# Kernel tuning notes

Measured on AMD Instinct MI355X. Metric: run time of the kernel, lower is better.

The kernel has to match this reference:

```python
import jax, jax.numpy as jnp
import numpy as np

D_IN = 200   # 4 * d_embeddings
H = 64       # hidden_size

def setup_inputs() -> dict:
    key = jax.random.key(0)
    ks = jax.random.split(key, 7)
    B, T = 4096, 128
    s_ih = 1.0 / np.sqrt(H)
    x = jax.random.normal(ks[0], (B, T, D_IN), dtype=jnp.float32)
    W_ih = jax.random.uniform(ks[1], (H, D_IN), minval=-s_ih, maxval=s_ih, dtype=jnp.float32)
    W_hh = jax.random.uniform(ks[2], (H, H), minval=-s_ih, maxval=s_ih, dtype=jnp.float32)
    b_ih = jax.random.uniform(ks[3], (H,), minval=-s_ih, maxval=s_ih, dtype=jnp.float32)
    b_hh = jax.random.uniform(ks[4], (H,), minval=-s_ih, maxval=s_ih, dtype=jnp.float32)
    W_out = jax.random.uniform(ks[5], (1, H), minval=-s_ih, maxval=s_ih, dtype=jnp.float32)
    b_out = jax.random.uniform(ks[6], (1,), minval=-s_ih, maxval=s_ih, dtype=jnp.float32)
    return {"x": x, "W_ih": W_ih, "W_hh": W_hh, "b_ih": b_ih, "b_hh": b_hh,
            "W_out": W_out, "b_out": b_out}

def reference(x, W_ih, W_hh, b_ih, b_hh, W_out, b_out):
    B = x.shape[0]
    # precompute input projection for all timesteps: [B, T, H]
    xp = jnp.einsum('btd,hd->bth', x, W_ih) + b_ih + b_hh
    def step(h, xt):
        h = jnp.tanh(xt + h @ W_hh.T)
        return h, None
    h0 = jnp.zeros((B, H), dtype=x.dtype)
    h_last, _ = jax.lax.scan(step, h0, jnp.swapaxes(xp, 0, 1))  # scan over time
    return jax.nn.sigmoid(h_last @ W_out.T + b_out)  # [B, 1]
```

## Files before the change

kernel.cpp:

```cpp
#include <hip/hip_runtime.h>
#include <hip/hip_bf16.h>


#define TSEQ 128
#define DIN  200
#define HID  64
#define NB   16
#define TC   4
#define NCH  (TSEQ/TC)

typedef short bf16x8 __attribute__((ext_vector_type(8)));
typedef float f32x4  __attribute__((ext_vector_type(4)));

__device__ __forceinline__ short f2bf(float f) {
  __hip_bfloat16 h = __float2bfloat16(f);
  return __builtin_bit_cast(short, h);
}
__device__ __forceinline__ bf16x8 cvt8(f32x4 a, f32x4 b) {
  bf16x8 r;
#pragma unroll
  for (int i = 0; i < 4; ++i) { r[i] = f2bf(a[i]); r[4 + i] = f2bf(b[i]); }
  return r;
}
__device__ __forceinline__ float fast_tanh(float x) {
  x = fminf(10.f, fmaxf(-10.f, x));
  float e = __expf(2.f * x);
  return (e - 1.f) * __builtin_amdgcn_rcpf(e + 1.f);
}
__device__ __forceinline__ void barrier_lds() {
  asm volatile("s_waitcnt lgkmcnt(0)" ::: "memory");
  __builtin_amdgcn_s_barrier();
  asm volatile("" ::: "memory");
}

__global__ __launch_bounds__(256, 1) void rnn_fused(
    const float* __restrict__ x,   const float* __restrict__ Wih,
    const float* __restrict__ Whh, const float* __restrict__ bih,
    const float* __restrict__ bhh, const float* __restrict__ Wout,
    const float* __restrict__ bout, float* __restrict__ out)
{
  __shared__ float          xp[TC][NB][68];
  __shared__ unsigned short hbuf[2][NB][72];

  const int tid  = threadIdx.x;
  const int w    = tid >> 6;
  const int lane = tid & 63;
  const int m    = lane & 15;
  const int g    = lane >> 4;
  const int b0   = blockIdx.x * NB;

  f32x4 pre[7][2];
  {
    const float* xrow = x + ((size_t)(b0 + m) * TSEQ + w) * DIN;
#pragma unroll
    for (int ks = 0; ks < 7; ++ks) {
      const int d = ks * 32 + g * 8;
      if (d < DIN) {
        pre[ks][0] = *reinterpret_cast<const f32x4*>(xrow + d);
        pre[ks][1] = *reinterpret_cast<const f32x4*>(xrow + d + 4);
      } else {
        pre[ks][0] = (f32x4)0.f; pre[ks][1] = (f32x4)0.f;
      }
    }
  }

  bf16x8 wihf[4][7];
#pragma unroll
  for (int nt = 0; nt < 4; ++nt) {
    const float* wr = Wih + (size_t)(nt * 16 + m) * DIN;
#pragma unroll
    for (int ks = 0; ks < 7; ++ks) {
      const int d = ks * 32 + g * 8;
      if (d < DIN) {
        f32x4 u0 = *reinterpret_cast<const f32x4*>(wr + d);
        f32x4 u1 = *reinterpret_cast<const f32x4*>(wr + d + 4);
        wihf[nt][ks] = cvt8(u0, u1);
      } else {
        wihf[nt][ks] = (bf16x8)0;
      }
    }
  }
  bf16x8 whhf[2];
#pragma unroll
  for (int ks = 0; ks < 2; ++ks) {
    const float* wr = Whh + (size_t)(w * 16 + m) * HID + ks * 32 + g * 8;
    f32x4 u0 = *reinterpret_cast<const f32x4*>(wr);
    f32x4 u1 = *reinterpret_cast<const f32x4*>(wr + 4);
    whhf[ks] = cvt8(u0, u1);
  }
  float bias[4];
#pragma unroll
  for (int nt = 0; nt < 4; ++nt) bias[nt] = bih[nt * 16 + m] + bhh[nt * 16 + m];

  for (int i = tid; i < NB * 72; i += 256) hbuf[1][0][i] = 0;
  barrier_lds();

  for (int c = 0; c < NCH; ++c) {
    bf16x8 afr[7];
#pragma unroll
    for (int ks = 0; ks < 7; ++ks) afr[ks] = cvt8(pre[ks][0], pre[ks][1]);

    if (c + 1 < NCH) {
      const float* xrow = x + ((size_t)(b0 + m) * TSEQ + ((c + 1) * TC + w)) * DIN;
#pragma unroll
      for (int ks = 0; ks < 7; ++ks) {
        const int d = ks * 32 + g * 8;
        if (d < DIN) {
          pre[ks][0] = *reinterpret_cast<const f32x4*>(xrow + d);
          pre[ks][1] = *reinterpret_cast<const f32x4*>(xrow + d + 4);
        }
      }
    }

    f32x4 acc[4];
#pragma unroll
    for (int nt = 0; nt < 4; ++nt) acc[nt] = (f32x4)(bias[nt]);
#pragma unroll
    for (int ks = 0; ks < 7; ++ks)
#pragma unroll
      for (int nt = 0; nt < 4; ++nt)
        acc[nt] = __builtin_amdgcn_mfma_f32_16x16x32_bf16(afr[ks], wihf[nt][ks], acc[nt], 0, 0, 0);

#pragma unroll
    for (int nt = 0; nt < 4; ++nt)
#pragma unroll
      for (int r = 0; r < 4; ++r)
        xp[w][g * 4 + r][nt * 16 + m] = acc[nt][r];
    barrier_lds();

#pragma unroll
    for (int tl = 0; tl < TC; ++tl) {
      const int tt = c * TC + tl;
      const int rb = tt & 1, pb = rb ^ 1;

      bf16x8 ha0 = *reinterpret_cast<const bf16x8*>(&hbuf[pb][m][g * 8]);
      bf16x8 ha1 = *reinterpret_cast<const bf16x8*>(&hbuf[pb][m][32 + g * 8]);

      f32x4 racc;
#pragma unroll
      for (int r = 0; r < 4; ++r) racc[r] = xp[tl][g * 4 + r][w * 16 + m];

      racc = __builtin_amdgcn_mfma_f32_16x16x32_bf16(ha0, whhf[0], racc, 0, 0, 0);
      racc = __builtin_amdgcn_mfma_f32_16x16x32_bf16(ha1, whhf[1], racc, 0, 0, 0);

#pragma unroll
      for (int r = 0; r < 4; ++r) {
        const float hv = fast_tanh(racc[r]);
        hbuf[rb][g * 4 + r][w * 16 + m] = (unsigned short)f2bf(hv);
        if (tt == TSEQ - 1) xp[0][g * 4 + r][w * 16 + m] = hv;
      }
      barrier_lds();
    }
  }

  if (tid < 64) {
    const int b = m, q = g;
    float s = 0.f;
#pragma unroll
    for (int j = 0; j < 16; ++j) s += xp[0][b][q * 16 + j] * Wout[q * 16 + j];
    s += __shfl_xor(s, 16, 64);
    s += __shfl_xor(s, 32, 64);
    if (q == 0) {
      const float z = s + bout[0];
      out[b0 + b] = 1.f / (1.f + __expf(-z));
    }
  }
}

extern "C" void kernel_launch(void* const* d_in, const int* in_sizes, int n_in,
                              void* d_out, int out_size, void* d_ws, size_t ws_size,
                              hipStream_t stream) {
  const float* x    = (const float*)d_in[0];
  const float* Wih  = (const float*)d_in[1];
  const float* Whh  = (const float*)d_in[2];
  const float* bih  = (const float*)d_in[3];
  const float* bhh  = (const float*)d_in[4];
  const float* Wout = (const float*)d_in[5];
  const float* bout = (const float*)d_in[6];
  float* out = (float*)d_out;

  const int B = in_sizes[0] / (TSEQ * DIN);
  rnn_fused<<<dim3(B / NB), dim3(256), 0, stream>>>(x, Wih, Whh, bih, bhh, Wout, bout, out);
}
```

Measured before the change: 101.6 us.

## Give each wavefront its own batch rows to drop block barriers; deepen x prefetch

Each wavefront now owns 4 batch rows and runs the full 64-wide recurrence itself, instead of four waves sharing 16 rows. Hidden state and the projected inputs stay in wave-private LDS, so every per-timestep block barrier goes away. The cost is 8 recurrent MFMAs per step instead of 2, with 3/4 of the A rows duplicated. The x loads are double-buffered two chunks ahead, tanh is rewritten as exp2 plus rcp, and the output reduction uses shuffles only.

```diff
diff --git a/kernel.cpp b/kernel.cpp
--- a/kernel.cpp
+++ b/kernel.cpp
@@ -5,7 +5,6 @@
 #define TSEQ 128
 #define DIN  200
 #define HID  64
-#define NB   16
 #define TC   4
 #define NCH  (TSEQ/TC)
 
@@ -22,15 +21,10 @@
   for (int i = 0; i < 4; ++i) { r[i] = f2bf(a[i]); r[4 + i] = f2bf(b[i]); }
   return r;
 }
-__device__ __forceinline__ float fast_tanh(float x) {
-  x = fminf(10.f, fmaxf(-10.f, x));
-  float e = __expf(2.f * x);
-  return (e - 1.f) * __builtin_amdgcn_rcpf(e + 1.f);
-}
-__device__ __forceinline__ void barrier_lds() {
-  asm volatile("s_waitcnt lgkmcnt(0)" ::: "memory");
-  __builtin_amdgcn_s_barrier();
-  asm volatile("" ::: "memory");
+__device__ __forceinline__ float tanh_fast(float x) {
+  float e = exp2f(x * 2.885390081777927f);
+  float r = __builtin_amdgcn_rcpf(1.f + e);
+  return __builtin_fmaf(-2.f, r, 1.f);
 }
 
 __global__ __launch_bounds__(256, 1) void rnn_fused(
@@ -39,30 +33,34 @@
     const float* __restrict__ bhh, const float* __restrict__ Wout,
     const float* __restrict__ bout, float* __restrict__ out)
 {
-  __shared__ float          xp[TC][NB][68];
-  __shared__ unsigned short hbuf[2][NB][72];
+  __shared__ float          xps[4][TC][HID][4];
+  __shared__ unsigned short hb [4][4][HID];
 
   const int tid  = threadIdx.x;
   const int w    = tid >> 6;
   const int lane = tid & 63;
   const int m    = lane & 15;
   const int g    = lane >> 4;
-  const int b0   = blockIdx.x * NB;
+  const int bw   = blockIdx.x * 16 + w * 4;
 
-  f32x4 pre[7][2];
-  {
-    const float* xrow = x + ((size_t)(b0 + m) * TSEQ + w) * DIN;
+  const float* xrow = x + ((size_t)(bw + (m >> 2)) * TSEQ + (m & 3)) * DIN;
+
+  f32x4 pA[7][2], pB[7][2];
+  auto LOADC = [&](f32x4 (&P)[7][2], int c) {
+    const float* p = xrow + (size_t)c * (TC * DIN);
 #pragma unroll
     for (int ks = 0; ks < 7; ++ks) {
       const int d = ks * 32 + g * 8;
-      if (d < DIN) {
-        pre[ks][0] = *reinterpret_cast<const f32x4*>(xrow + d);
-        pre[ks][1] = *reinterpret_cast<const f32x4*>(xrow + d + 4);
+      if (d + 8 <= DIN) {
+        P[ks][0] = *reinterpret_cast<const f32x4*>(p + d);
+        P[ks][1] = *reinterpret_cast<const f32x4*>(p + d + 4);
       } else {
-        pre[ks][0] = (f32x4)0.f; pre[ks][1] = (f32x4)0.f;
+        P[ks][0] = (f32x4)0.f; P[ks][1] = (f32x4)0.f;
       }
     }
-  }
+  };
+  LOADC(pA, 0);
+  LOADC(pB, 1);
 
   bf16x8 wihf[4][7];
 #pragma unroll
@@ -71,50 +69,42 @@
 #pragma unroll
     for (int ks = 0; ks < 7; ++ks) {
       const int d = ks * 32 + g * 8;
-      if (d < DIN) {
-        f32x4 u0 = *reinterpret_cast<const f32x4*>(wr + d);
-        f32x4 u1 = *reinterpret_cast<const f32x4*>(wr + d + 4);
-        wihf[nt][ks] = cvt8(u0, u1);
-      } else {
+      if (d + 8 <= DIN)
+        wihf[nt][ks] = cvt8(*reinterpret_cast<const f32x4*>(wr + d),
+                            *reinterpret_cast<const f32x4*>(wr + d + 4));
+      else
         wihf[nt][ks] = (bf16x8)0;
-      }
     }
   }
-  bf16x8 whhf[2];
+  bf16x8 whhf[4][2];
 #pragma unroll
-  for (int ks = 0; ks < 2; ++ks) {
-    const float* wr = Whh + (size_t)(w * 16 + m) * HID + ks * 32 + g * 8;
-    f32x4 u0 = *reinterpret_cast<const f32x4*>(wr);
-    f32x4 u1 = *reinterpret_cast<const f32x4*>(wr + 4);
-    whhf[ks] = cvt8(u0, u1);
-  }
-  float bias[4];
+  for (int nt = 0; nt < 4; ++nt)
 #pragma unroll
-  for (int nt = 0; nt < 4; ++nt) bias[nt] = bih[nt * 16 + m] + bhh[nt * 16 + m];
+    for (int hf = 0; hf < 2; ++hf) {
+      const float* wr = Whh + (size_t)(nt * 16 + m) * HID + hf * 32 + g * 8;
+      whhf[nt][hf] = cvt8(*reinterpret_cast<const f32x4*>(wr),
+                          *reinterpret_cast<const f32x4*>(wr + 4));
+    }
+  float biasv[4];
+#pragma unroll
+  for (int nt = 0; nt < 4; ++nt) biasv[nt] = bih[nt * 16 + m] + bhh[nt * 16 + m];
+  const float woutv = Wout[g * 16 + m];
+  const float bout0 = bout[0];
 
-  for (int i = tid; i < NB * 72; i += 256) hbuf[1][0][i] = 0;
-  barrier_lds();
+  reinterpret_cast<unsigned int*>(&hb[w][0][0])[lane]      = 0u;
+  reinterpret_cast<unsigned int*>(&hb[w][0][0])[lane + 64] = 0u;
 
-  for (int c = 0; c < NCH; ++c) {
+  float vf[4];
+
+  auto BODY = [&](f32x4 (&P)[7][2], int c) {
     bf16x8 afr[7];
 #pragma unroll
-    for (int ks = 0; ks < 7; ++ks) afr[ks] = cvt8(pre[ks][0], pre[ks][1]);
-
-    if (c + 1 < NCH) {
-      const float* xrow = x + ((size_t)(b0 + m) * TSEQ + ((c + 1) * TC + w)) * DIN;
-#pragma unroll
-      for (int ks = 0; ks < 7; ++ks) {
-        const int d = ks * 32 + g * 8;
-        if (d < DIN) {
-          pre[ks][0] = *reinterpret_cast<const f32x4*>(xrow + d);
-          pre[ks][1] = *reinterpret_cast<const f32x4*>(xrow + d + 4);
-        }
-      }
-    }
+    for (int ks = 0; ks < 7; ++ks) afr[ks] = cvt8(P[ks][0], P[ks][1]);
+    if (c + 2 < NCH) LOADC(P, c + 2);
 
     f32x4 acc[4];
 #pragma unroll
-    for (int nt = 0; nt < 4; ++nt) acc[nt] = (f32x4)(bias[nt]);
+    for (int nt = 0; nt < 4; ++nt) acc[nt] = (f32x4)(biasv[nt]);
 #pragma unroll
     for (int ks = 0; ks < 7; ++ks)
 #pragma unroll
@@ -124,46 +114,51 @@
 #pragma unroll
     for (int nt = 0; nt < 4; ++nt)
 #pragma unroll
-      for (int r = 0; r < 4; ++r)
-        xp[w][g * 4 + r][nt * 16 + m] = acc[nt][r];
-    barrier_lds();
+      for (int rr = 0; rr < 4; ++rr)
+        xps[w][rr][nt * 16 + m][g] = acc[nt][rr];
 
 #pragma unroll
     for (int tl = 0; tl < TC; ++tl) {
-      const int tt = c * TC + tl;
-      const int rb = tt & 1, pb = rb ^ 1;
-
-      bf16x8 ha0 = *reinterpret_cast<const bf16x8*>(&hbuf[pb][m][g * 8]);
-      bf16x8 ha1 = *reinterpret_cast<const bf16x8*>(&hbuf[pb][m][32 + g * 8]);
-
-      f32x4 racc;
+      f32x4 racc[4];
 #pragma unroll
-      for (int r = 0; r < 4; ++r) racc[r] = xp[tl][g * 4 + r][w * 16 + m];
-
-      racc = __builtin_amdgcn_mfma_f32_16x16x32_bf16(ha0, whhf[0], racc, 0, 0, 0);
-      racc = __builtin_amdgcn_mfma_f32_16x16x32_bf16(ha1, whhf[1], racc, 0, 0, 0);
-
+      for (int nt = 0; nt < 4; ++nt)
+        racc[nt] = *reinterpret_cast<const f32x4*>(&xps[w][tl][nt * 16 + m][0]);
+      bf16x8 ha0 = *reinterpret_cast<const bf16x8*>(&hb[w][m & 3][g * 8]);
+      bf16x8 ha1 = *reinterpret_cast<const bf16x8*>(&hb[w][m & 3][32 + g * 8]);
+#pragma unroll
+      for (int nt = 0; nt < 4; ++nt) {
+        racc[nt] = __builtin_amdgcn_mfma_f32_16x16x32_bf16(ha0, whhf[nt][0], racc[nt], 0, 0, 0);
+        racc[nt] = __builtin_amdgcn_mfma_f32_16x16x32_bf16(ha1, whhf[nt][1], racc[nt], 0, 0, 0);
+      }
 #pragma unroll
       for (int r = 0; r < 4; ++r) {
-        const float hv = fast_tanh(racc[r]);
-        hbuf[rb][g * 4 + r][w * 16 + m] = (unsigned short)f2bf(hv);
-        if (tt == TSEQ - 1) xp[0][g * 4 + r][w * 16 + m] = hv;
+        float v = (g == 0) ? racc[0][r] : (g == 1) ? racc[1][r]
+                 : (g == 2) ? racc[2][r] : racc[3][r];
+        v = tanh_fast(v);
+        vf[r] = v;
+        hb[w][r][g * 16 + m] = (unsigned short)f2bf(v);
       }
-      barrier_lds();
     }
+  };
+
+  for (int c = 0; c < NCH; c += 2) { BODY(pA, c); BODY(pB, c + 1); }
+
+  f32x4 s;
+#pragma unroll
+  for (int r = 0; r < 4; ++r) s[r] = vf[r] * woutv;
+#pragma unroll
+  for (int mask = 1; mask < 64; mask <<= 1) {
+#pragma unroll
+    for (int r = 0; r < 4; ++r) s[r] += __shfl_xor(s[r], mask, 64);
   }
-
-  if (tid < 64) {
-    const int b = m, q = g;
-    float s = 0.f;
+  if (lane == 0) {
+    f32x4 o;
 #pragma unroll
-    for (int j = 0; j < 16; ++j) s += xp[0][b][q * 16 + j] * Wout[q * 16 + j];
-    s += __shfl_xor(s, 16, 64);
-    s += __shfl_xor(s, 32, 64);
-    if (q == 0) {
-      const float z = s + bout[0];
-      out[b0 + b] = 1.f / (1.f + __expf(-z));
+    for (int r = 0; r < 4; ++r) {
+      const float z = s[r] + bout0;
+      o[r] = __builtin_amdgcn_rcpf(1.f + exp2f(-z * 1.4426950408889634f));
     }
+    *reinterpret_cast<f32x4*>(out + bw) = o;
   }
 }
 
@@ -180,5 +175,5 @@
   float* out = (float*)d_out;
 
   const int B = in_sizes[0] / (TSEQ * DIN);
-  rnn_fused<<<dim3(B / NB), dim3(256), 0, stream>>>(x, Wih, Whh, bih, bhh, Wout, bout, out);
+  rnn_fused<<<dim3(B / 16), dim3(256), 0, stream>>>(x, Wih, Whh, bih, bhh, Wout, bout, out);
 }
```

Result: slower. 106.3 us (+4.6%).

## Halve batch tile, stage x via async global_load_lds double-buffer, run two blocks per CU

Applied to the files above, without the earlier changes.

The batch tile drops from 16 to 8 rows per block so twice as many blocks launch, and launch bounds now allow two blocks per CU. Input chunks are copied straight into a double-buffered LDS staging area with global_load_lds, waited on with explicit vmcnt, replacing the old register prefetch. The 16-row MFMA tiles stay the same size, so half of each tile is padding whose results are thrown away. tanh is also simplified to an exp2 plus reciprocal form without clamping.

```diff
diff --git a/kernel.cpp b/kernel.cpp
--- a/kernel.cpp
+++ b/kernel.cpp
@@ -5,42 +5,54 @@
 #define TSEQ 128
 #define DIN  200
 #define HID  64
-#define NB   16
+#define NB   8
 #define TC   4
 #define NCH  (TSEQ/TC)
+#define RSTRIDE 804
 
 typedef short bf16x8 __attribute__((ext_vector_type(8)));
 typedef float f32x4  __attribute__((ext_vector_type(4)));
-
-__device__ __forceinline__ short f2bf(float f) {
+typedef const __attribute__((address_space(1))) unsigned int GU32;
+typedef __attribute__((address_space(3))) unsigned int LU32;
+
+__device__ __forceinline__ unsigned short f2bf(float f) {
   __hip_bfloat16 h = __float2bfloat16(f);
-  return __builtin_bit_cast(short, h);
+  return __builtin_bit_cast(unsigned short, h);
 }
 __device__ __forceinline__ bf16x8 cvt8(f32x4 a, f32x4 b) {
   bf16x8 r;
 #pragma unroll
-  for (int i = 0; i < 4; ++i) { r[i] = f2bf(a[i]); r[4 + i] = f2bf(b[i]); }
+  for (int i = 0; i < 4; ++i) { r[i] = (short)f2bf(a[i]); r[4 + i] = (short)f2bf(b[i]); }
   return r;
 }
-__device__ __forceinline__ float fast_tanh(float x) {
-  x = fminf(10.f, fmaxf(-10.f, x));
-  float e = __expf(2.f * x);
-  return (e - 1.f) * __builtin_amdgcn_rcpf(e + 1.f);
+__device__ __forceinline__ float tanh_fast(float x) {
+  float e = exp2f(x * 2.885390081777927f);
+  float r = __builtin_amdgcn_rcpf(1.f + e);
+  return __builtin_fmaf(-2.f, r, 1.f);
 }
 __device__ __forceinline__ void barrier_lds() {
   asm volatile("s_waitcnt lgkmcnt(0)" ::: "memory");
   __builtin_amdgcn_s_barrier();
-  asm volatile("" ::: "memory");
-}
-
-__global__ __launch_bounds__(256, 1) void rnn_fused(
+  __builtin_amdgcn_sched_barrier(0);
+}
+__device__ __forceinline__ void wait_vm8() {
+  asm volatile("s_waitcnt vmcnt(8)" ::: "memory");
+  __builtin_amdgcn_sched_barrier(0);
+}
+__device__ __forceinline__ void wait_vm0() {
+  asm volatile("s_waitcnt vmcnt(0)" ::: "memory");
+  __builtin_amdgcn_sched_barrier(0);
+}
+
+__global__ __launch_bounds__(256, 2) void rnn_fused(
     const float* __restrict__ x,   const float* __restrict__ Wih,
     const float* __restrict__ Whh, const float* __restrict__ bih,
     const float* __restrict__ bhh, const float* __restrict__ Wout,
     const float* __restrict__ bout, float* __restrict__ out)
 {
+  __shared__ float          stg[2][NB][RSTRIDE];
   __shared__ float          xp[TC][NB][68];
-  __shared__ unsigned short hbuf[2][NB][72];
+  __shared__ unsigned short hbuf[2][16][72];
 
   const int tid  = threadIdx.x;
   const int w    = tid >> 6;
@@ -49,120 +61,127 @@
   const int g    = lane >> 4;
   const int b0   = blockIdx.x * NB;
 
-  f32x4 pre[7][2];
-  {
-    const float* xrow = x + ((size_t)(b0 + m) * TSEQ + w) * DIN;
+  bf16x8 wihf[4][7];
+#pragma unroll
+  for (int nt = 0; nt < 4; ++nt) {
+    const float* wr = Wih + (size_t)(nt * 16 + m) * DIN;
 #pragma unroll
     for (int ks = 0; ks < 7; ++ks) {
       const int d = ks * 32 + g * 8;
-      if (d < DIN) {
-        pre[ks][0] = *reinterpret_cast<const f32x4*>(xrow + d);
-        pre[ks][1] = *reinterpret_cast<const f32x4*>(xrow + d + 4);
-      } else {
-        pre[ks][0] = (f32x4)0.f; pre[ks][1] = (f32x4)0.f;
+      if (d + 8 <= DIN)
+        wihf[nt][ks] = cvt8(*reinterpret_cast<const f32x4*>(wr + d),
+                            *reinterpret_cast<const f32x4*>(wr + d + 4));
+      else
+        wihf[nt][ks] = (bf16x8)0;
+    }
+  }
+  bf16x8 whhf[2];
+#pragma unroll
+  for (int hf = 0; hf < 2; ++hf) {
+    const float* wr = Whh + (size_t)(w * 16 + m) * HID + hf * 32 + g * 8;
+    whhf[hf] = cvt8(*reinterpret_cast<const f32x4*>(wr),
+                    *reinterpret_cast<const f32x4*>(wr + 4));
+  }
+  float biasv[4];
+#pragma unroll
+  for (int nt = 0; nt < 4; ++nt) biasv[nt] = bih[nt * 16 + m] + bhh[nt * 16 + m];
+
+  wait_vm0();
+
+  auto LOADC = [&](int buf, int c) {
+#pragma unroll
+    for (int r = 0; r < 2; ++r) {
+      const int row = w * 2 + r;
+      const float* gb = x + (size_t)(b0 + row) * (TSEQ * DIN) + (size_t)c * (TC * DIN);
+      float* lb = &stg[buf][row][0];
+#pragma unroll
+      for (int i = 0; i < 3; ++i)
+        __builtin_amdgcn_global_load_lds((GU32*)(gb + i * 256 + lane * 4),
+                                         (LU32*)(lb + i * 256), 16, 0, 0);
+      if (lane < 8)
+        __builtin_amdgcn_global_load_lds((GU32*)(gb + 768 + lane * 4),
+                                         (LU32*)(lb + 768), 16, 0, 0);
+    }
+  };
+  LOADC(0, 0);
+  LOADC(1, 1);
+
+  for (int i = tid; i < 2 * 16 * 72 / 2; i += 256)
+    reinterpret_cast<unsigned int*>(&hbuf[0][0][0])[i] = 0u;
+
+  for (int c = 0; c < NCH; ++c) {
+    const int buf = c & 1;
+    if (c + 1 < NCH) wait_vm8(); else wait_vm0();
+    __builtin_amdgcn_s_barrier();
+    __builtin_amdgcn_sched_barrier(0);
+
+    bf16x8 afr[7];
+    {
+      const float* sp = &stg[buf][0][0];
+#pragma unroll
+      for (int ks = 0; ks < 7; ++ks) {
+        const int off = m * RSTRIDE + w * 200 + (ks < 6 ? ks * 32 + g * 8 : 192);
+        afr[ks] = cvt8(*reinterpret_cast<const f32x4*>(sp + off),
+                       *reinterpret_cast<const f32x4*>(sp + off + 4));
       }
-    }
-  }
-
-  bf16x8 wihf[4][7];
-#pragma unroll
-  for (int nt = 0; nt < 4; ++nt) {
-    const float* wr = Wih + (size_t)(nt * 16 + m) * DIN;
-#pragma unroll
-    for (int ks = 0; ks < 7; ++ks) {
-      const int d = ks * 32 + g * 8;
-      if (d < DIN) {
-        f32x4 u0 = *reinterpret_cast<const f32x4*>(wr + d);
-        f32x4 u1 = *reinterpret_cast<const f32x4*>(wr + d + 4);
-        wihf[nt][ks] = cvt8(u0, u1);
-      } else {
-        wihf[nt][ks] = (bf16x8)0;
-      }
-    }
-  }
-  bf16x8 whhf[2];
-#pragma unroll
-  for (int ks = 0; ks < 2; ++ks) {
-    const float* wr = Whh + (size_t)(w * 16 + m) * HID + ks * 32 + g * 8;
-    f32x4 u0 = *reinterpret_cast<const f32x4*>(wr);
-    f32x4 u1 = *reinterpret_cast<const f32x4*>(wr + 4);
-    whhf[ks] = cvt8(u0, u1);
-  }
-  float bias[4];
-#pragma unroll
-  for (int nt = 0; nt < 4; ++nt) bias[nt] = bih[nt * 16 + m] + bhh[nt * 16 + m];
-
-  for (int i = tid; i < NB * 72; i += 256) hbuf[1][0][i] = 0;
-  barrier_lds();
-
-  for (int c = 0; c < NCH; ++c) {
-    bf16x8 afr[7];
-#pragma unroll
-    for (int ks = 0; ks < 7; ++ks) afr[ks] = cvt8(pre[ks][0], pre[ks][1]);
-
-    if (c + 1 < NCH) {
-      const float* xrow = x + ((size_t)(b0 + m) * TSEQ + ((c + 1) * TC + w)) * DIN;
-#pragma unroll
-      for (int ks = 0; ks < 7; ++ks) {
-        const int d = ks * 32 + g * 8;
-        if (d < DIN) {
-          pre[ks][0] = *reinterpret_cast<const f32x4*>(xrow + d);
-          pre[ks][1] = *reinterpret_cast<const f32x4*>(xrow + d + 4);
-        }
-      }
-    }
+      if (g != 0) afr[6] = (bf16x8)0;
+    }
+    barrier_lds();
+
+    if (c + 2 < NCH) LOADC(buf, c + 2);
 
     f32x4 acc[4];
 #pragma unroll
-    for (int nt = 0; nt < 4; ++nt) acc[nt] = (f32x4)(bias[nt]);
+    for (int nt = 0; nt < 4; ++nt) acc[nt] = (f32x4)(biasv[nt]);
 #pragma unroll
     for (int ks = 0; ks < 7; ++ks)
 #pragma unroll
       for (int nt = 0; nt < 4; ++nt)
         acc[nt] = __builtin_amdgcn_mfma_f32_16x16x32_bf16(afr[ks], wihf[nt][ks], acc[nt], 0, 0, 0);
-
-#pragma unroll
-    for (int nt = 0; nt < 4; ++nt)
-#pragma unroll
-      for (int r = 0; r < 4; ++r)
-        xp[w][g * 4 + r][nt * 16 + m] = acc[nt][r];
+    if (g < 2) {
+#pragma unroll
+      for (int nt = 0; nt < 4; ++nt)
+#pragma unroll
+        for (int rr = 0; rr < 4; ++rr)
+          xp[w][g * 4 + rr][nt * 16 + m] = acc[nt][rr];
+    }
     barrier_lds();
 
 #pragma unroll
     for (int tl = 0; tl < TC; ++tl) {
       const int tt = c * TC + tl;
       const int rb = tt & 1, pb = rb ^ 1;
-
       bf16x8 ha0 = *reinterpret_cast<const bf16x8*>(&hbuf[pb][m][g * 8]);
       bf16x8 ha1 = *reinterpret_cast<const bf16x8*>(&hbuf[pb][m][32 + g * 8]);
-
       f32x4 racc;
 #pragma unroll
       for (int r = 0; r < 4; ++r) racc[r] = xp[tl][g * 4 + r][w * 16 + m];
-
       racc = __builtin_amdgcn_mfma_f32_16x16x32_bf16(ha0, whhf[0], racc, 0, 0, 0);
       racc = __builtin_amdgcn_mfma_f32_16x16x32_bf16(ha1, whhf[1], racc, 0, 0, 0);
-
-#pragma unroll
-      for (int r = 0; r < 4; ++r) {
-        const float hv = fast_tanh(racc[r]);
-        hbuf[rb][g * 4 + r][w * 16 + m] = (unsigned short)f2bf(hv);
-        if (tt == TSEQ - 1) xp[0][g * 4 + r][w * 16 + m] = hv;
+      if (g < 2) {
+#pragma unroll
+        for (int r = 0; r < 4; ++r) {
+          const float hv = tanh_fast(racc[r]);
+          hbuf[rb][g * 4 + r][w * 16 + m] = f2bf(hv);
+          if (tt == TSEQ - 1) xp[0][g * 4 + r][w * 16 + m] = hv;
+        }
       }
       barrier_lds();
     }
   }
 
   if (tid < 64) {
-    const int b = m, q = g;
+    const int b  = lane >> 3;
+    const int j0 = (lane & 7) * 8;
     float s = 0.f;
 #pragma unroll
-    for (int j = 0; j < 16; ++j) s += xp[0][b][q * 16 + j] * Wout[q * 16 + j];
-    s += __shfl_xor(s, 16, 64);
-    s += __shfl_xor(s, 32, 64);
-    if (q == 0) {
+    for (int j = 0; j < 8; ++j) s += xp[0][b][j0 + j] * Wout[j0 + j];
+    s += __shfl_xor(s, 1, 64);
+    s += __shfl_xor(s, 2, 64);
+    s += __shfl_xor(s, 4, 64);
+    if ((lane & 7) == 0) {
       const float z = s + bout[0];
-      out[b0 + b] = 1.f / (1.f + __expf(-z));
+      out[b0 + b] = __builtin_amdgcn_rcpf(1.f + exp2f(-z * 1.4426950408889634f));
     }
   }
 }
```

Result: faster. 98.18 us, median of 2 (-3.3%).
